# Kernel optimization log

Hardware: AMD Instinct MI355X
Metric: run time of the kernel (lower is better)

## Reference

```python
import jax, jax.numpy as jnp
import numpy as np

N, E, DM, H, DFF = 20000, 640000, 512, 8, 2048
DK = DM // H


def _layernorm(x, g, b, eps=1e-5):
    mu = jnp.mean(x, axis=-1, keepdims=True)
    var = jnp.mean(jnp.square(x - mu), axis=-1, keepdims=True)
    return (x - mu) * jax.lax.rsqrt(var + eps) * g + b


def setup_inputs() -> dict:
    key = jax.random.key(0)
    ks = jax.random.split(key, 12)
    s = 0.02
    h = jax.random.normal(ks[0], (N, DM), dtype=jnp.float32)
    src = jax.random.randint(ks[1], (E,), 0, N, dtype=jnp.int32)
    dst = jnp.sort(jax.random.randint(ks[2], (E,), 0, N, dtype=jnp.int32))
    return {
        "h": h,
        "src": src,
        "dst": dst,
        "Wq": jax.random.normal(ks[3], (DM, DM), dtype=jnp.float32) * s,
        "Wk": jax.random.normal(ks[4], (DM, DM), dtype=jnp.float32) * s,
        "Wv": jax.random.normal(ks[5], (DM, DM), dtype=jnp.float32) * s,
        "Wo": jax.random.normal(ks[6], (DM, DM), dtype=jnp.float32) * s,
        "ln1_g": jnp.ones((DM,), jnp.float32),
        "ln1_b": jnp.zeros((DM,), jnp.float32),
        "ln2_g": jnp.ones((DM,), jnp.float32),
        "ln2_b": jnp.zeros((DM,), jnp.float32),
        "W1": jax.random.normal(ks[7], (DM, DFF), dtype=jnp.float32) * s,
        "b1": jnp.zeros((DFF,), jnp.float32),
        "W2": jax.random.normal(ks[8], (DFF, DM), dtype=jnp.float32) * s,
        "b2": jnp.zeros((DM,), jnp.float32),
    }


def reference(h, src, dst, Wq, Wk, Wv, Wo, ln1_g, ln1_b, ln2_g, ln2_b, W1, b1, W2, b2):
    n = h.shape[0]
    # q/k/v projections (MaskedMMCSR equivalent score: k[src] . q[dst])
    q = (h @ Wq).reshape(n, H, DK)
    k = (h @ Wk).reshape(n, H, DK)
    v = (h @ Wv).reshape(n, H, DK)
    e = jnp.einsum("ehd,ehd->eh", k[src], q[dst]) / np.sqrt(DK).astype(np.float32)  # [E,H]
    # SparseSoftmax: softmax over incoming edges of each dst node
    m = jax.ops.segment_max(e, dst, num_segments=n)  # [n,H]
    ex = jnp.exp(e - m[dst])
    z = jax.ops.segment_sum(ex, dst, num_segments=n)
    attn = ex / z[dst]  # [E,H]
    # VectorSPMM: a[dst] = sum_e attn[e] * v[src[e]]
    a = jax.ops.segment_sum(attn[:, :, None] * v[src], dst, num_segments=n)
    a = a.reshape(n, DM)
    o = a @ Wo
    x = _layernorm(h + o, ln1_g, ln1_b)
    f = jax.nn.relu(x @ W1 + b1) @ W2 + b2
    return _layernorm(x + f, ln2_g, ln2_b)
```

## Files before the change

kernel.cpp:

```cpp
#include <hip/hip_runtime.h>
#include <cstdint>
#include <cstddef>

#define DMODEL 512
#define NHEAD 8
#define DFFN 2048
#define CHUNK 256

typedef float  floatx4  __attribute__((ext_vector_type(4)));
typedef short  shortx8  __attribute__((ext_vector_type(8)));
typedef unsigned short ushortx4 __attribute__((ext_vector_type(4)));
typedef unsigned short ushortx8 __attribute__((ext_vector_type(8)));

__device__ __forceinline__ float bf2f(unsigned short u) {
  union { unsigned int i; float f; } v; v.i = ((unsigned int)u) << 16; return v.f;
}
__device__ __forceinline__ unsigned short f2bf(float x) {
  union { float f; unsigned int i; } v; v.f = x;
  unsigned int r = v.i + 0x7fffu + ((v.i >> 16) & 1u);
  return (unsigned short)(r >> 16);
}

__device__ __forceinline__ void gload_lds16(const unsigned short* g, unsigned short* l) {
  __builtin_amdgcn_global_load_lds(
      (const __attribute__((address_space(1))) void*)g,
      (__attribute__((address_space(3))) void*)l,
      16, 0, 0);
}


__global__ void k_cast_bf16(const float* __restrict__ in, unsigned short* __restrict__ out, int n4)
{
  const int i = blockIdx.x * blockDim.x + threadIdx.x;
  if (i >= n4) return;
  const floatx4 v = *(const floatx4*)(in + (size_t)i * 4);
  ushortx4 o;
#pragma unroll
  for (int j = 0; j < 4; ++j) o[j] = f2bf(v[j]);
  *(ushortx4*)(out + (size_t)i * 4) = o;
}

__global__ void k_transpose_cast(const float* __restrict__ W, unsigned short* __restrict__ out, int K, int Nn)
{
  const int idx = blockIdx.x * blockDim.x + threadIdx.x;
  if (idx >= K * Nn) return;
  const int k = idx / Nn, n = idx - k * Nn;
  out[(size_t)n * K + k] = f2bf(W[idx]);
}

__global__ void k_row_ptr(const int* __restrict__ dst, int* __restrict__ rowp, int N_, int E_)
{
  const int i = blockIdx.x * blockDim.x + threadIdx.x;
  if (i > N_) return;
  int lo = 0, hi = E_;
  while (lo < hi) { const int mid = (lo + hi) >> 1; if (dst[mid] < i) lo = mid + 1; else hi = mid; }
  rowp[i] = lo;
}


template <typename OutT, bool HAS_BIAS, bool RELU>
__global__ __launch_bounds__(256) void k_gemm(
    const unsigned short* __restrict__ A,
    const unsigned short* __restrict__ BT,
    OutT* __restrict__ C,
    const float* __restrict__ bias,
    int M, int Nn, int K)
{
  __shared__ __align__(16) unsigned short As[128 * 64];
  __shared__ __align__(16) unsigned short Bs[128 * 64];
  const int tid  = threadIdx.x;
  const int wid  = tid >> 6;
  const int lane = tid & 63;
  const int wm = wid >> 1, wn = wid & 1;
  const int m0 = blockIdx.x * 128, n0 = blockIdx.y * 128;

  floatx4 acc[4][4];
#pragma unroll
  for (int i = 0; i < 4; ++i)
#pragma unroll
    for (int j = 0; j < 4; ++j) acc[i][j] = (floatx4)(0.0f);

  const int srow  = tid >> 3;
  const int scolb = ((tid & 7) ^ (srow & 7)) * 8;
  const int fr = lane & 15;
  const int fb = lane >> 4;
  const int fx = fr & 7;

  const int arow[4] = { (wm * 64 +  0 + fr) * 64, (wm * 64 + 16 + fr) * 64,
                        (wm * 64 + 32 + fr) * 64, (wm * 64 + 48 + fr) * 64 };
  const int brow[4] = { (wn * 64 +  0 + fr) * 64, (wn * 64 + 16 + fr) * 64,
                        (wn * 64 + 32 + fr) * 64, (wn * 64 + 48 + fr) * 64 };

  for (int k0 = 0; k0 < K; k0 += 64) {
#pragma unroll
    for (int r = 0; r < 4; ++r) {
      int ra = m0 + r * 32 + srow;
      if (ra > M - 1) ra = M - 1;
      gload_lds16(A + (size_t)ra * K + k0 + scolb, &As[r * 2048 + tid * 8]);
    }
#pragma unroll
    for (int r = 0; r < 4; ++r) {
      const int rb = n0 + r * 32 + srow;
      gload_lds16(BT + (size_t)rb * K + k0 + scolb, &Bs[r * 2048 + tid * 8]);
    }
    __syncthreads();

#pragma unroll
    for (int kk = 0; kk < 2; ++kk) {
      const int blk = ((kk * 4 + fb) ^ fx) * 8;
      shortx8 af[4], bfr[4];
#pragma unroll
      for (int i = 0; i < 4; ++i) af[i]  = *(const shortx8*)&As[arow[i] + blk];
#pragma unroll
      for (int j = 0; j < 4; ++j) bfr[j] = *(const shortx8*)&Bs[brow[j] + blk];
#pragma unroll
      for (int i = 0; i < 4; ++i)
#pragma unroll
        for (int j = 0; j < 4; ++j)
          acc[i][j] = __builtin_amdgcn_mfma_f32_16x16x32_bf16(af[i], bfr[j], acc[i][j], 0, 0, 0);
    }
    __syncthreads();
  }

  const int cr = (lane >> 4) * 4;
  const int cc = lane & 15;
#pragma unroll
  for (int j = 0; j < 4; ++j) {
    const int col = n0 + wn * 64 + j * 16 + cc;
    float bv = 0.0f;
    if (HAS_BIAS) bv = bias[col];
#pragma unroll
    for (int i = 0; i < 4; ++i) {
      const int rb = m0 + wm * 64 + i * 16 + cr;
#pragma unroll
      for (int r = 0; r < 4; ++r) {
        const int row = rb + r;
        if (row < M) {
          float v = acc[i][j][r];
          if (HAS_BIAS) v += bv;
          if (RELU) v = fmaxf(v, 0.0f);
          if constexpr (sizeof(OutT) == 2) C[(size_t)row * Nn + col] = f2bf(v);
          else                             C[(size_t)row * Nn + col] = v;
        }
      }
    }
  }
}


__global__ __launch_bounds__(256) void k_attn_fused(
    const unsigned short* __restrict__ qkv,
    const int* __restrict__ src, const int* __restrict__ rowp,
    unsigned short* __restrict__ a_bf, int N_)
{
  const int n = blockIdx.x;
  const int tid = threadIdx.x;
  const int wv = tid >> 6, lane = tid & 63;
  const int r0 = rowp[n], r1 = rowp[n + 1];
  const int deg = r1 - r0;

  __shared__ int   s_src[CHUNK];
  __shared__ float s_raw[CHUNK * NHEAD];

  float qr[8];
  {
    const ushortx8 qf = *(const ushortx8*)(qkv + (size_t)n * 1536 + lane * 8);
#pragma unroll
    for (int i = 0; i < 8; ++i) qr[i] = bf2f(qf[i]);
  }

  const int head = lane >> 3, sub = lane & 7;
  const int hh = tid >> 5;
  const int d0 = tid * 2;

  float a0 = 0.0f, a1 = 0.0f, z = 0.0f;

  for (int c0 = 0; c0 < deg; c0 += CHUNK) {
    const int clen = min(CHUNK, deg - c0);

    if (tid < clen) s_src[tid] = src[r0 + c0 + tid];
    __syncthreads();

    for (int i = wv; i < clen; i += 8) {
      const int i1 = (i + 4 < clen) ? i + 4 : i;
      const int s0 = s_src[i], s1 = s_src[i1];
      const ushortx8 kf0 = *(const ushortx8*)(qkv + (size_t)s0 * 1536 + 512 + lane * 8);
      const ushortx8 kf1 = *(const ushortx8*)(qkv + (size_t)s1 * 1536 + 512 + lane * 8);
      float acc0 = 0.0f, acc1 = 0.0f;
#pragma unroll
      for (int t = 0; t < 8; ++t) acc0 += qr[t] * bf2f(kf0[t]);
#pragma unroll
      for (int t = 0; t < 8; ++t) acc1 += qr[t] * bf2f(kf1[t]);
      acc0 += __shfl_xor(acc0, 1); acc1 += __shfl_xor(acc1, 1);
      acc0 += __shfl_xor(acc0, 2); acc1 += __shfl_xor(acc1, 2);
      acc0 += __shfl_xor(acc0, 4); acc1 += __shfl_xor(acc1, 4);
      if (sub == 0) {
        s_raw[i * 8 + head] = __expf(acc0 * 0.125f);
        if (i1 != i) s_raw[i1 * 8 + head] = __expf(acc1 * 0.125f);
      }
    }
    __syncthreads();

    const unsigned short* vbase = qkv + 1024 + d0;
    int j = 0;
    for (; j + 4 <= clen; j += 4) {
      const unsigned int v0 = *(const unsigned int*)(vbase + (size_t)s_src[j]     * 1536);
      const unsigned int v1 = *(const unsigned int*)(vbase + (size_t)s_src[j + 1] * 1536);
      const unsigned int v2 = *(const unsigned int*)(vbase + (size_t)s_src[j + 2] * 1536);
      const unsigned int v3 = *(const unsigned int*)(vbase + (size_t)s_src[j + 3] * 1536);
      const float p0 = s_raw[(j)     * 8 + hh];
      const float p1 = s_raw[(j + 1) * 8 + hh];
      const float p2 = s_raw[(j + 2) * 8 + hh];
      const float p3 = s_raw[(j + 3) * 8 + hh];
      a0 += p0 * bf2f((unsigned short)(v0 & 0xffffu));
      a1 += p0 * bf2f((unsigned short)(v0 >> 16));
      a0 += p1 * bf2f((unsigned short)(v1 & 0xffffu));
      a1 += p1 * bf2f((unsigned short)(v1 >> 16));
      a0 += p2 * bf2f((unsigned short)(v2 & 0xffffu));
      a1 += p2 * bf2f((unsigned short)(v2 >> 16));
      a0 += p3 * bf2f((unsigned short)(v3 & 0xffffu));
      a1 += p3 * bf2f((unsigned short)(v3 >> 16));
      z += p0 + p1 + p2 + p3;
    }
    for (; j < clen; ++j) {
      const unsigned int vv = *(const unsigned int*)(vbase + (size_t)s_src[j] * 1536);
      const float p = s_raw[j * 8 + hh];
      a0 += p * bf2f((unsigned short)(vv & 0xffffu));
      a1 += p * bf2f((unsigned short)(vv >> 16));
      z += p;
    }
    __syncthreads();
  }

  const float invz = (z > 0.0f) ? 1.0f / z : 0.0f;
  const unsigned int lo = f2bf(a0 * invz);
  const unsigned int hi = f2bf(a1 * invz);
  *(unsigned int*)(a_bf + (size_t)n * 512 + d0) = lo | (hi << 16);
}


template <bool WRITE_BF>
__global__ __launch_bounds__(256) void k_ln(
    const float* __restrict__ xa, const float* __restrict__ xb,
    const float* __restrict__ g, const float* __restrict__ b,
    float* __restrict__ out_f, unsigned short* __restrict__ out_bf, int n_rows)
{
  const int row = blockIdx.x * 4 + (threadIdx.x >> 6);
  if (row >= n_rows) return;
  const int lane = threadIdx.x & 63;
  const float* pa = xa + (size_t)row * DMODEL + lane * 8;
  const float* pb = xb + (size_t)row * DMODEL + lane * 8;
  float v[8];
  {
    floatx4 a0 = *(const floatx4*)pa;
    floatx4 a1 = *(const floatx4*)(pa + 4);
    floatx4 b0 = *(const floatx4*)pb;
    floatx4 b1 = *(const floatx4*)(pb + 4);
#pragma unroll
    for (int j = 0; j < 4; ++j) { v[j] = a0[j] + b0[j]; v[4 + j] = a1[j] + b1[j]; }
  }
  float s = 0.0f;
#pragma unroll
  for (int j = 0; j < 8; ++j) s += v[j];
#pragma unroll
  for (int d = 1; d < 64; d <<= 1) s += __shfl_xor(s, d);
  const float mu = s * (1.0f / DMODEL);
  float q = 0.0f;
#pragma unroll
  for (int j = 0; j < 8; ++j) { const float t = v[j] - mu; q += t * t; }
#pragma unroll
  for (int d = 1; d < 64; d <<= 1) q += __shfl_xor(q, d);
  const float rs = rsqrtf(q * (1.0f / DMODEL) + 1e-5f);
  const float* gp = g + lane * 8;
  const float* bp = b + lane * 8;
  floatx4 g0 = *(const floatx4*)gp, g1 = *(const floatx4*)(gp + 4);
  floatx4 h0 = *(const floatx4*)bp, h1 = *(const floatx4*)(bp + 4);
  float o[8];
#pragma unroll
  for (int j = 0; j < 4; ++j) {
    o[j]     = (v[j]     - mu) * rs * g0[j] + h0[j];
    o[4 + j] = (v[4 + j] - mu) * rs * g1[j] + h1[j];
  }
  float* po = out_f + (size_t)row * DMODEL + lane * 8;
  *(floatx4*)po       = (floatx4){o[0], o[1], o[2], o[3]};
  *(floatx4*)(po + 4) = (floatx4){o[4], o[5], o[6], o[7]};
  if (WRITE_BF) {
    ushortx8 ob;
#pragma unroll
    for (int j = 0; j < 8; ++j) ob[j] = f2bf(o[j]);
    *(ushortx8*)(out_bf + (size_t)row * DMODEL + lane * 8) = ob;
  }
}


extern "C" void kernel_launch(void* const* d_in, const int* in_sizes, int n_in,
                              void* d_out, int out_size, void* d_ws, size_t ws_size,
                              hipStream_t stream)
{
  (void)n_in; (void)out_size; (void)ws_size;
  const float* h    = (const float*)d_in[0];
  const int*   src  = (const int*)  d_in[1];
  const int*   dst  = (const int*)  d_in[2];
  const float* Wq   = (const float*)d_in[3];
  const float* Wk   = (const float*)d_in[4];
  const float* Wv   = (const float*)d_in[5];
  const float* Wo   = (const float*)d_in[6];
  const float* ln1g = (const float*)d_in[7];
  const float* ln1b = (const float*)d_in[8];
  const float* ln2g = (const float*)d_in[9];
  const float* ln2b = (const float*)d_in[10];
  const float* W1   = (const float*)d_in[11];
  const float* b1   = (const float*)d_in[12];
  const float* W2   = (const float*)d_in[13];
  const float* b2   = (const float*)d_in[14];

  const int N_ = in_sizes[0] / DMODEL;
  const int E_ = in_sizes[1];

  char* ws = (char*)d_ws;
  size_t off = 0;
  auto alloc = [&](size_t bytes) -> void* {
    void* p = ws + off;
    off += (bytes + 255) & ~(size_t)255;
    return p;
  };

  char* regA = (char*)alloc((size_t)N_ * DMODEL * 2);
  char* regB = (char*)alloc((size_t)N_ * DFFN * 2);
  char* regC = (char*)alloc((size_t)N_ * DMODEL * 4);
  char* regD = (char*)alloc((size_t)N_ * DMODEL * 2);
  char* regE = (char*)alloc((size_t)N_ * DMODEL * 4);

  unsigned short* qkvT  = (unsigned short*)alloc((size_t)1536 * 512 * 2);
  unsigned short* WoT   = (unsigned short*)alloc((size_t)512 * 512 * 2);
  unsigned short* W1T   = (unsigned short*)alloc((size_t)2048 * 512 * 2);
  unsigned short* W2T   = (unsigned short*)alloc((size_t)512 * 2048 * 2);
  int*            rowp  = (int*)alloc((size_t)(N_ + 1) * 4);

  unsigned short* h_bf  = (unsigned short*)regA;
  unsigned short* qkv   = (unsigned short*)regB;
  unsigned short* midbf = (unsigned short*)regB;
  float*          o     = (float*)regC;
  float*          f     = (float*)regC;
  unsigned short* a_bf  = (unsigned short*)regD;
  unsigned short* x_bf  = (unsigned short*)regD;
  float*          x     = (float*)regE;

  {
    const int n4 = N_ * DMODEL / 4;
    k_cast_bf16<<<(n4 + 255) / 256, 256, 0, stream>>>(h, h_bf, n4);
  }
  k_transpose_cast<<<(512 * 512 + 255) / 256, 256, 0, stream>>>(Wq, qkvT + 0 * 512 * 512, 512, 512);
  k_transpose_cast<<<(512 * 512 + 255) / 256, 256, 0, stream>>>(Wk, qkvT + 1 * 512 * 512, 512, 512);
  k_transpose_cast<<<(512 * 512 + 255) / 256, 256, 0, stream>>>(Wv, qkvT + 2 * 512 * 512, 512, 512);
  k_transpose_cast<<<(512 * 512 + 255) / 256, 256, 0, stream>>>(Wo, WoT, 512, 512);
  k_transpose_cast<<<(512 * 2048 + 255) / 256, 256, 0, stream>>>(W1, W1T, 512, 2048);
  k_transpose_cast<<<(512 * 2048 + 255) / 256, 256, 0, stream>>>(W2, W2T, 2048, 512);
  k_row_ptr<<<(N_ + 1 + 255) / 256, 256, 0, stream>>>(dst, rowp, N_, E_);

  const int mt = (N_ + 127) / 128;
  k_gemm<unsigned short, false, false><<<dim3(mt, 1536 / 128), 256, 0, stream>>>(h_bf, qkvT, qkv, nullptr, N_, 1536, 512);
  k_attn_fused<<<N_, 256, 0, stream>>>(qkv, src, rowp, a_bf, N_);
  k_gemm<float, false, false><<<dim3(mt, 512 / 128), 256, 0, stream>>>(a_bf, WoT, o, nullptr, N_, 512, 512);
  k_ln<true><<<(N_ + 3) / 4, 256, 0, stream>>>(h, o, ln1g, ln1b, x, x_bf, N_);
  k_gemm<unsigned short, true, true><<<dim3(mt, 2048 / 128), 256, 0, stream>>>(x_bf, W1T, midbf, b1, N_, 2048, 512);
  k_gemm<float, true, false><<<dim3(mt, 512 / 128), 256, 0, stream>>>(midbf, W2T, f, b2, N_, 512, 2048);
  k_ln<false><<<(N_ + 3) / 4, 256, 0, stream>>>(x, f, ln2g, ln2b, (float*)d_out, nullptr, N_);
}
```

Before: 615.2 us.

## Process each destination node with one wavefront in a single pass over edges

The attention kernel moves from one 256-thread block per node, with shared-memory staging, two barrier-separated phases and chunking, to one 64-lane wavefront per node with four nodes per block. Each lane now loads K and V for four edges at once, computes the scores with shuffles, and accumulates exp-weighted V in registers. This removes shared memory, __syncthreads and the block-size overhead for low-degree nodes (average degree about 32). The cost is less parallelism per node and more register use for the four-edge unroll, and the softmax still applies no max subtraction.

```diff
diff --git a/kernel.cpp b/kernel.cpp
--- a/kernel.cpp
+++ b/kernel.cpp
@@ -5,7 +5,6 @@
 #define DMODEL 512
 #define NHEAD 8
 #define DFFN 2048
-#define CHUNK 256
 
 typedef float  floatx4  __attribute__((ext_vector_type(4)));
 typedef short  shortx8  __attribute__((ext_vector_type(8)));
@@ -148,19 +147,16 @@
 }
 
 
-__global__ __launch_bounds__(256) void k_attn_fused(
+__global__ __launch_bounds__(256) void k_attn_wave(
     const unsigned short* __restrict__ qkv,
     const int* __restrict__ src, const int* __restrict__ rowp,
     unsigned short* __restrict__ a_bf, int N_)
 {
-  const int n = blockIdx.x;
-  const int tid = threadIdx.x;
-  const int wv = tid >> 6, lane = tid & 63;
+  const int n = blockIdx.x * 4 + (threadIdx.x >> 6);
+  if (n >= N_) return;
+  const int lane = threadIdx.x & 63;
+
   const int r0 = rowp[n], r1 = rowp[n + 1];
-  const int deg = r1 - r0;
-
-  __shared__ int   s_src[CHUNK];
-  __shared__ float s_raw[CHUNK * NHEAD];
 
   float qr[8];
   {
@@ -169,73 +165,63 @@
     for (int i = 0; i < 8; ++i) qr[i] = bf2f(qf[i]);
   }
 
-  const int head = lane >> 3, sub = lane & 7;
-  const int hh = tid >> 5;
-  const int d0 = tid * 2;
-
-  float a0 = 0.0f, a1 = 0.0f, z = 0.0f;
-
-  for (int c0 = 0; c0 < deg; c0 += CHUNK) {
-    const int clen = min(CHUNK, deg - c0);
-
-    if (tid < clen) s_src[tid] = src[r0 + c0 + tid];
-    __syncthreads();
-
-    for (int i = wv; i < clen; i += 8) {
-      const int i1 = (i + 4 < clen) ? i + 4 : i;
-      const int s0 = s_src[i], s1 = s_src[i1];
-      const ushortx8 kf0 = *(const ushortx8*)(qkv + (size_t)s0 * 1536 + 512 + lane * 8);
-      const ushortx8 kf1 = *(const ushortx8*)(qkv + (size_t)s1 * 1536 + 512 + lane * 8);
-      float acc0 = 0.0f, acc1 = 0.0f;
-#pragma unroll
-      for (int t = 0; t < 8; ++t) acc0 += qr[t] * bf2f(kf0[t]);
-#pragma unroll
-      for (int t = 0; t < 8; ++t) acc1 += qr[t] * bf2f(kf1[t]);
-      acc0 += __shfl_xor(acc0, 1); acc1 += __shfl_xor(acc1, 1);
-      acc0 += __shfl_xor(acc0, 2); acc1 += __shfl_xor(acc1, 2);
-      acc0 += __shfl_xor(acc0, 4); acc1 += __shfl_xor(acc1, 4);
-      if (sub == 0) {
-        s_raw[i * 8 + head] = __expf(acc0 * 0.125f);
-        if (i1 != i) s_raw[i1 * 8 + head] = __expf(acc1 * 0.125f);
-      }
-    }
-    __syncthreads();
-
-    const unsigned short* vbase = qkv + 1024 + d0;
-    int j = 0;
-    for (; j + 4 <= clen; j += 4) {
-      const unsigned int v0 = *(const unsigned int*)(vbase + (size_t)s_src[j]     * 1536);
-      const unsigned int v1 = *(const unsigned int*)(vbase + (size_t)s_src[j + 1] * 1536);
-      const unsigned int v2 = *(const unsigned int*)(vbase + (size_t)s_src[j + 2] * 1536);
-      const unsigned int v3 = *(const unsigned int*)(vbase + (size_t)s_src[j + 3] * 1536);
-      const float p0 = s_raw[(j)     * 8 + hh];
-      const float p1 = s_raw[(j + 1) * 8 + hh];
-      const float p2 = s_raw[(j + 2) * 8 + hh];
-      const float p3 = s_raw[(j + 3) * 8 + hh];
-      a0 += p0 * bf2f((unsigned short)(v0 & 0xffffu));
-      a1 += p0 * bf2f((unsigned short)(v0 >> 16));
-      a0 += p1 * bf2f((unsigned short)(v1 & 0xffffu));
-      a1 += p1 * bf2f((unsigned short)(v1 >> 16));
-      a0 += p2 * bf2f((unsigned short)(v2 & 0xffffu));
-      a1 += p2 * bf2f((unsigned short)(v2 >> 16));
-      a0 += p3 * bf2f((unsigned short)(v3 & 0xffffu));
-      a1 += p3 * bf2f((unsigned short)(v3 >> 16));
-      z += p0 + p1 + p2 + p3;
-    }
-    for (; j < clen; ++j) {
-      const unsigned int vv = *(const unsigned int*)(vbase + (size_t)s_src[j] * 1536);
-      const float p = s_raw[j * 8 + hh];
-      a0 += p * bf2f((unsigned short)(vv & 0xffffu));
-      a1 += p * bf2f((unsigned short)(vv >> 16));
-      z += p;
-    }
-    __syncthreads();
+  float av[8];
+#pragma unroll
+  for (int i = 0; i < 8; ++i) av[i] = 0.0f;
+  float z = 0.0f;
+
+  const unsigned short* kbase = qkv + 512  + lane * 8;
+  const unsigned short* vbase = qkv + 1024 + lane * 8;
+
+  for (int j = r0; j < r1; j += 4) {
+    const int nb = r1 - j;
+    const int e1 = (nb > 1) ? j + 1 : j;
+    const int e2 = (nb > 2) ? j + 2 : j;
+    const int e3 = (nb > 3) ? j + 3 : j;
+    const int s0 = src[j], s1 = src[e1], s2 = src[e2], s3 = src[e3];
+
+    const ushortx8 kf0 = *(const ushortx8*)(kbase + (size_t)s0 * 1536);
+    const ushortx8 kf1 = *(const ushortx8*)(kbase + (size_t)s1 * 1536);
+    const ushortx8 kf2 = *(const ushortx8*)(kbase + (size_t)s2 * 1536);
+    const ushortx8 kf3 = *(const ushortx8*)(kbase + (size_t)s3 * 1536);
+    const ushortx8 vf0 = *(const ushortx8*)(vbase + (size_t)s0 * 1536);
+    const ushortx8 vf1 = *(const ushortx8*)(vbase + (size_t)s1 * 1536);
+    const ushortx8 vf2 = *(const ushortx8*)(vbase + (size_t)s2 * 1536);
+    const ushortx8 vf3 = *(const ushortx8*)(vbase + (size_t)s3 * 1536);
+
+    float c0 = 0.0f, c1 = 0.0f, c2 = 0.0f, c3 = 0.0f;
+#pragma unroll
+    for (int t = 0; t < 8; ++t) c0 += qr[t] * bf2f(kf0[t]);
+#pragma unroll
+    for (int t = 0; t < 8; ++t) c1 += qr[t] * bf2f(kf1[t]);
+#pragma unroll
+    for (int t = 0; t < 8; ++t) c2 += qr[t] * bf2f(kf2[t]);
+#pragma unroll
+    for (int t = 0; t < 8; ++t) c3 += qr[t] * bf2f(kf3[t]);
+#pragma unroll
+    for (int m = 1; m <= 4; m <<= 1) {
+      c0 += __shfl_xor(c0, m);
+      c1 += __shfl_xor(c1, m);
+      c2 += __shfl_xor(c2, m);
+      c3 += __shfl_xor(c3, m);
+    }
+    const float p0 = __expf(c0 * 0.125f);
+    const float p1 = (nb > 1) ? __expf(c1 * 0.125f) : 0.0f;
+    const float p2 = (nb > 2) ? __expf(c2 * 0.125f) : 0.0f;
+    const float p3 = (nb > 3) ? __expf(c3 * 0.125f) : 0.0f;
+
+#pragma unroll
+    for (int t = 0; t < 8; ++t)
+      av[t] += p0 * bf2f(vf0[t]) + p1 * bf2f(vf1[t])
+             + p2 * bf2f(vf2[t]) + p3 * bf2f(vf3[t]);
+    z += p0 + p1 + p2 + p3;
   }
 
   const float invz = (z > 0.0f) ? 1.0f / z : 0.0f;
-  const unsigned int lo = f2bf(a0 * invz);
-  const unsigned int hi = f2bf(a1 * invz);
-  *(unsigned int*)(a_bf + (size_t)n * 512 + d0) = lo | (hi << 16);
+  ushortx8 ob;
+#pragma unroll
+  for (int t = 0; t < 8; ++t) ob[t] = f2bf(av[t] * invz);
+  *(ushortx8*)(a_bf + (size_t)n * 512 + lane * 8) = ob;
 }
 
 
@@ -360,7 +346,7 @@
 
   const int mt = (N_ + 127) / 128;
   k_gemm<unsigned short, false, false><<<dim3(mt, 1536 / 128), 256, 0, stream>>>(h_bf, qkvT, qkv, nullptr, N_, 1536, 512);
-  k_attn_fused<<<N_, 256, 0, stream>>>(qkv, src, rowp, a_bf, N_);
+  k_attn_wave<<<(N_ + 3) / 4, 256, 0, stream>>>(qkv, src, rowp, a_bf, N_);
   k_gemm<float, false, false><<<dim3(mt, 512 / 128), 256, 0, stream>>>(a_bf, WoT, o, nullptr, N_, 512, 512);
   k_ln<true><<<(N_ + 3) / 4, 256, 0, stream>>>(h, o, ln1g, ln1b, x, x_bf, N_);
   k_gemm<unsigned short, true, true><<<dim3(mt, 2048 / 128), 256, 0, stream>>>(x_bf, W1T, midbf, b1, N_, 2048, 512);
```

Result: no change. 614.7 us (-0.1%).
